# Kernel optimization log

Measured on AMD Instinct MI355X. Metric: run time of the kernel, lower is better.

Reference implementation:

```python
import jax, jax.numpy as jnp
import numpy as np

N_NODES = 100000
N_EDGES = 1600000
IN_FEATS = 128
OUT_FEATS = 256
K = 32


def setup_inputs() -> dict:
    key = jax.random.key(0)
    ks = jax.random.split(key, 8)
    feat = jax.random.normal(ks[0], (N_NODES, IN_FEATS), dtype=jnp.float32)
    # MaxK sparsified activations: nonnegative values (post-ReLU top-k)
    topk_values = jax.random.uniform(ks[1], (N_NODES, K), dtype=jnp.float32)
    topk_indices = jax.random.randint(ks[2], (N_NODES, K), 0, IN_FEATS, dtype=jnp.int32)
    # CSR expanded to COO: sorted row ids emulate indptr ordering
    row = jnp.sort(jax.random.randint(ks[3], (N_EDGES,), 0, N_NODES, dtype=jnp.int32))
    col = jax.random.randint(ks[4], (N_EDGES,), 0, N_NODES, dtype=jnp.int32)
    # in-degrees clamped to min 1.0, as in set_graph_data
    deg = jax.ops.segment_sum(jnp.ones((N_EDGES,), jnp.float32), row, num_segments=N_NODES)
    degrees = jnp.maximum(deg, 1.0)
    gain = float(np.sqrt(2.0))  # calculate_gain('relu')
    bnd_n = gain * np.sqrt(6.0 / (IN_FEATS + OUT_FEATS))
    W_neigh = jax.random.uniform(ks[5], (IN_FEATS, OUT_FEATS), jnp.float32, -bnd_n, bnd_n)
    W_self = jax.random.uniform(ks[6], (IN_FEATS, OUT_FEATS), jnp.float32, -bnd_n, bnd_n)
    bnd_b = 1.0 / np.sqrt(IN_FEATS)
    b_self = jax.random.uniform(ks[7], (OUT_FEATS,), jnp.float32, -bnd_b, bnd_b)
    return {"feat": feat, "topk_values": topk_values, "topk_indices": topk_indices,
            "row": row, "col": col, "degrees": degrees,
            "W_neigh": W_neigh, "W_self": W_self, "b_self": b_self}


def reference(feat, topk_values, topk_indices, row, col, degrees, W_neigh, W_self, b_self):
    n = feat.shape[0]
    # Scatter top-k sparse features back to dense [N, in_feats]
    # (real top-k indices are unique per row, so add == set; add is deterministic)
    rows = jnp.arange(n, dtype=jnp.int32)[:, None]
    x_sparse = jnp.zeros((n, IN_FEATS), feat.dtype).at[rows, topk_indices].add(topk_values)
    # CSR SpMM with all-ones edge values + degree normalization (mean aggregation)
    gathered = x_sparse[col]                                  # [E, in_feats]
    agg = jax.ops.segment_sum(gathered, row, num_segments=n)  # [N, in_feats]
    agg = agg / degrees[:, None]
    # lin_before_mp is False (in_feats <= out_feats): linear after aggregation
    h_neigh = agg @ W_neigh                                    # [N, out_feats]
    rst = feat @ W_self + b_self + h_neigh
    return rst
```

## Files before the change

### kernel.cpp

```cpp
#include <hip/hip_runtime.h>
#include <hip/hip_bf16.h>
#include <stdint.h>

#define IN_FEATS 128
#define OUT_FEATS 256
#define TOPK 32
#define BM 128
#define BN 128
#define BK 32
#define AL 40
#define KTOT 256

typedef float f32x4 __attribute__((ext_vector_type(4)));
typedef short bf16x8 __attribute__((ext_vector_type(8)));

__device__ __forceinline__ unsigned short f2bf(float x) {
    unsigned u = __float_as_uint(x);
    u += 0x7FFFu + ((u >> 16) & 1u);
    return (unsigned short)(u >> 16);
}

__global__ void k_scatter(const float* __restrict__ vals, const int* __restrict__ idxs,
                          unsigned short* __restrict__ xsp, int n_nodes) {
    __shared__ float lds[2 * IN_FEATS];
    int t = threadIdx.x;
    int n0 = blockIdx.x * 2;
    lds[t] = 0.f;
    __syncthreads();
    if (t < 2 * TOPK) {
        int h = t >> 5;
        int k = t & 31;
        int n = n0 + h;
        if (n < n_nodes) {
            float v = vals[(size_t)n * TOPK + k];
            int ix = idxs[(size_t)n * TOPK + k];
            atomicAdd(&lds[h * IN_FEATS + ix], v);
        }
    }
    __syncthreads();
    int h2 = t >> 7;
    int f = t & 127;
    int n = n0 + h2;
    if (n < n_nodes) xsp[(size_t)n * IN_FEATS + f] = f2bf(lds[t]);
}

__global__ void k_weights(const float* __restrict__ Wn, const float* __restrict__ Ws,
                          unsigned short* __restrict__ WT) {
    int idx = blockIdx.x * 256 + threadIdx.x;
    int n = idx >> 8;
    int k = idx & 255;
    float v = (k < IN_FEATS) ? Wn[(size_t)k * OUT_FEATS + n]
                             : Ws[(size_t)(k - IN_FEATS) * OUT_FEATS + n];
    WT[idx] = f2bf(v);
}

__global__ void k_indptr(const int* __restrict__ row, int* __restrict__ indptr,
                         int n_nodes, int n_edges) {
    int e = blockIdx.x * 256 + threadIdx.x;
    if (e >= n_edges) return;
    int r = row[e];
    int rp = (e == 0) ? -1 : row[e - 1];
    for (int x = rp + 1; x <= r; ++x) indptr[x] = e;
    if (e == n_edges - 1)
        for (int x = r + 1; x <= n_nodes; ++x) indptr[x] = n_edges;
}

__global__ __launch_bounds__(256) void k_aggregate(
    const unsigned short* __restrict__ xsp,
    const int* __restrict__ indptr, const int* __restrict__ col,
    unsigned short* __restrict__ agg, int n_nodes) {
    int t = threadIdx.x;
    int node = blockIdx.x * 4 + (t >> 6);
    if (node >= n_nodes) return;
    int lane = t & 63;
    int eg = lane >> 4, fi = lane & 15;
    int e0 = indptr[node], e1 = indptr[node + 1];

    float acc[8] = {0.f, 0.f, 0.f, 0.f, 0.f, 0.f, 0.f, 0.f};
    int elast = (e1 > e0) ? (e1 - 1) : e0;
    for (int base = e0; base < e1; base += 8) {
        int ea = base + eg;
        int eb = base + 4 + eg;
        float sa = (ea < e1) ? 1.f : 0.f;
        float sb = (eb < e1) ? 1.f : 0.f;
        int ca = col[ea < elast ? ea : elast];
        int cb = col[eb < elast ? eb : elast];
        uint4 ua = *(const uint4*)(xsp + (size_t)ca * IN_FEATS + fi * 8);
        uint4 ub = *(const uint4*)(xsp + (size_t)cb * IN_FEATS + fi * 8);
        unsigned pa[4] = {ua.x, ua.y, ua.z, ua.w};
        unsigned pb[4] = {ub.x, ub.y, ub.z, ub.w};
#pragma unroll
        for (int i = 0; i < 4; ++i) {
            acc[2 * i]     = fmaf(sa, __uint_as_float(pa[i] << 16), acc[2 * i]);
            acc[2 * i + 1] = fmaf(sa, __uint_as_float(pa[i] & 0xFFFF0000u), acc[2 * i + 1]);
            acc[2 * i]     = fmaf(sb, __uint_as_float(pb[i] << 16), acc[2 * i]);
            acc[2 * i + 1] = fmaf(sb, __uint_as_float(pb[i] & 0xFFFF0000u), acc[2 * i + 1]);
        }
    }
#pragma unroll
    for (int i = 0; i < 8; ++i) {
        acc[i] += __shfl_down(acc[i], 16, 64);
        acc[i] += __shfl_down(acc[i], 32, 64);
    }
    if (eg == 0) {
        int cnt = e1 - e0;
        float inv = 1.0f / (float)(cnt > 0 ? cnt : 1);
        unsigned o[4];
#pragma unroll
        for (int i = 0; i < 4; ++i) {
            unsigned lo = f2bf(acc[2 * i] * inv);
            unsigned hi = f2bf(acc[2 * i + 1] * inv);
            o[i] = lo | (hi << 16);
        }
        *(uint4*)(agg + (size_t)node * IN_FEATS + fi * 8) = *(uint4*)&o[0];
    }
}

__global__ __launch_bounds__(256) void k_gemm(
    const unsigned short* __restrict__ agg,
    const float* __restrict__ feat,
    const unsigned short* __restrict__ WT,
    const float* __restrict__ bias,
    float* __restrict__ out, int n_nodes) {
    __shared__ __align__(16) unsigned short Ash[BM * AL];
    __shared__ __align__(16) unsigned short Bsh[BN * AL];
    int t = threadIdx.x;
    int m0 = blockIdx.x * BM;
    int n0 = blockIdx.y * BN;
    int lane = t & 63;
    int w = t >> 6;
    int wr = w >> 1, wc = w & 1;
    int lrow = lane & 15, quad = lane >> 4;

    f32x4 acc[4][4];
    for (int i = 0; i < 4; ++i)
        for (int j = 0; j < 4; ++j)
            acc[i][j] = (f32x4){0.f, 0.f, 0.f, 0.f};

    for (int kk = 0; kk < KTOT; kk += BK) {
        for (int pass = 0; pass < 2; ++pass) {
            int g = t + pass * 256;
            int rowi = g >> 2;
            int q = g & 3;
            int gk = kk + q * 8;
            int node = m0 + rowi;
            if (node >= n_nodes) node = n_nodes - 1;
            uint4 v;
            if (kk < IN_FEATS) {
                v = *(const uint4*)(agg + (size_t)node * IN_FEATS + gk);
            } else {
                const float* fp = feat + (size_t)node * IN_FEATS + (gk - IN_FEATS);
                float4 f0 = *(const float4*)fp;
                float4 f1 = *(const float4*)(fp + 4);
                v.x = (unsigned)f2bf(f0.x) | ((unsigned)f2bf(f0.y) << 16);
                v.y = (unsigned)f2bf(f0.z) | ((unsigned)f2bf(f0.w) << 16);
                v.z = (unsigned)f2bf(f1.x) | ((unsigned)f2bf(f1.y) << 16);
                v.w = (unsigned)f2bf(f1.z) | ((unsigned)f2bf(f1.w) << 16);
            }
            *(uint4*)&Ash[rowi * AL + q * 8] = v;

            uint4 bv = *(const uint4*)(WT + (size_t)(n0 + rowi) * KTOT + gk);
            *(uint4*)&Bsh[rowi * AL + q * 8] = bv;
        }
        __syncthreads();

        bf16x8 af[4], bfr[4];
        for (int mi = 0; mi < 4; ++mi)
            af[mi] = *(const bf16x8*)&Ash[(wr * 64 + mi * 16 + lrow) * AL + quad * 8];
        for (int ni = 0; ni < 4; ++ni)
            bfr[ni] = *(const bf16x8*)&Bsh[(wc * 64 + ni * 16 + lrow) * AL + quad * 8];
        for (int mi = 0; mi < 4; ++mi)
            for (int ni = 0; ni < 4; ++ni)
                acc[mi][ni] = __builtin_amdgcn_mfma_f32_16x16x32_bf16(
                    af[mi], bfr[ni], acc[mi][ni], 0, 0, 0);
        __syncthreads();
    }

    for (int mi = 0; mi < 4; ++mi) {
        int gm = m0 + wr * 64 + mi * 16 + quad * 4;
        for (int ni = 0; ni < 4; ++ni) {
            int go = n0 + wc * 64 + ni * 16 + lrow;
            float b = bias[go];
            for (int r = 0; r < 4; ++r) {
                int node = gm + r;
                if (node < n_nodes)
                    out[(size_t)node * OUT_FEATS + go] = acc[mi][ni][r] + b;
            }
        }
    }
}

extern "C" void kernel_launch(void* const* d_in, const int* in_sizes, int n_in,
                              void* d_out, int out_size, void* d_ws, size_t ws_size,
                              hipStream_t stream) {
    const float* feat = (const float*)d_in[0];
    const float* tkv  = (const float*)d_in[1];
    const int*   tki  = (const int*)d_in[2];
    const int*   row  = (const int*)d_in[3];
    const int*   col  = (const int*)d_in[4];
    const float* Wn   = (const float*)d_in[6];
    const float* Ws   = (const float*)d_in[7];
    const float* bias = (const float*)d_in[8];
    float* out = (float*)d_out;

    int n_nodes = in_sizes[5];
    int n_edges = in_sizes[3];

    unsigned short* xsp = (unsigned short*)d_ws;
    unsigned short* agg = xsp + (size_t)n_nodes * IN_FEATS;
    unsigned short* WT  = agg + (size_t)n_nodes * IN_FEATS;
    int* indptr = (int*)(WT + (size_t)OUT_FEATS * KTOT);

    k_scatter<<<(n_nodes + 1) / 2, 256, 0, stream>>>(tkv, tki, xsp, n_nodes);
    k_weights<<<256, 256, 0, stream>>>(Wn, Ws, WT);
    k_indptr<<<(n_edges + 255) / 256, 256, 0, stream>>>(row, indptr, n_nodes, n_edges);
    k_aggregate<<<(n_nodes + 3) / 4, 256, 0, stream>>>(xsp, indptr, col, agg, n_nodes);
    dim3 g3((n_nodes + BM - 1) / BM, OUT_FEATS / BN);
    k_gemm<<<g3, 256, 0, stream>>>(agg, feat, WT, bias, out, n_nodes);
}
```

Before: 304.3 us.

## Stage concatenated bf16 A matrix and use direct global-to-LDS loads in GEMM

The feat-to-bf16 conversion moves into the aggregation kernel, which writes a concatenated [agg | feat] bf16 matrix of row stride 256. The GEMM then loads A and B tiles with global_load_lds straight into XOR-swizzled LDS at BK=64, replacing register-staged loads, in-kernel conversion and padded LDS rows. This is meant to cut GEMM load instructions and fp32 feat traffic repeated across both N-blocks. In exchange it adds an extra bf16 write and read of feat through the workspace.

```diff
diff --git a/kernel.cpp b/kernel.cpp
--- a/kernel.cpp
+++ b/kernel.cpp
@@ -1,5 +1,4 @@
 #include <hip/hip_runtime.h>
-#include <hip/hip_bf16.h>
 #include <stdint.h>
 
 #define IN_FEATS 128
@@ -7,8 +6,7 @@
 #define TOPK 32
 #define BM 128
 #define BN 128
-#define BK 32
-#define AL 40
+#define BK 64
 #define KTOT 256
 
 typedef float f32x4 __attribute__((ext_vector_type(4)));
@@ -18,6 +16,12 @@
     unsigned u = __float_as_uint(x);
     u += 0x7FFFu + ((u >> 16) & 1u);
     return (unsigned short)(u >> 16);
+}
+
+__device__ __forceinline__ void gload16(const void* g, void* l) {
+    __builtin_amdgcn_global_load_lds(
+        (const __attribute__((address_space(1))) unsigned*)g,
+        (__attribute__((address_space(3))) unsigned*)l, 16, 0, 0);
 }
 
 __global__ void k_scatter(const float* __restrict__ vals, const int* __restrict__ idxs,
@@ -67,8 +71,9 @@
 
 __global__ __launch_bounds__(256) void k_aggregate(
     const unsigned short* __restrict__ xsp,
+    const float* __restrict__ feat,
     const int* __restrict__ indptr, const int* __restrict__ col,
-    unsigned short* __restrict__ agg, int n_nodes) {
+    unsigned short* __restrict__ Acat, int n_nodes) {
     int t = threadIdx.x;
     int node = blockIdx.x * 4 + (t >> 6);
     if (node >= n_nodes) return;
@@ -112,18 +117,20 @@
             unsigned hi = f2bf(acc[2 * i + 1] * inv);
             o[i] = lo | (hi << 16);
         }
-        *(uint4*)(agg + (size_t)node * IN_FEATS + fi * 8) = *(uint4*)&o[0];
-    }
+        *(uint4*)(Acat + (size_t)node * KTOT + fi * 8) = *(uint4*)&o[0];
+    }
+    float2 fv = *(const float2*)(feat + (size_t)node * IN_FEATS + lane * 2);
+    unsigned pk = (unsigned)f2bf(fv.x) | ((unsigned)f2bf(fv.y) << 16);
+    *(unsigned*)(Acat + (size_t)node * KTOT + IN_FEATS + lane * 2) = pk;
 }
 
 __global__ __launch_bounds__(256) void k_gemm(
-    const unsigned short* __restrict__ agg,
-    const float* __restrict__ feat,
+    const unsigned short* __restrict__ Acat,
     const unsigned short* __restrict__ WT,
     const float* __restrict__ bias,
     float* __restrict__ out, int n_nodes) {
-    __shared__ __align__(16) unsigned short Ash[BM * AL];
-    __shared__ __align__(16) unsigned short Bsh[BN * AL];
+    __shared__ __align__(16) unsigned short Ash[BM * BK];
+    __shared__ __align__(16) unsigned short Bsh[BN * BK];
     int t = threadIdx.x;
     int m0 = blockIdx.x * BM;
     int n0 = blockIdx.y * BN;
@@ -133,54 +140,58 @@
     int lrow = lane & 15, quad = lane >> 4;
 
     f32x4 acc[4][4];
+#pragma unroll
     for (int i = 0; i < 4; ++i)
+#pragma unroll
         for (int j = 0; j < 4; ++j)
             acc[i][j] = (f32x4){0.f, 0.f, 0.f, 0.f};
 
     for (int kk = 0; kk < KTOT; kk += BK) {
-        for (int pass = 0; pass < 2; ++pass) {
-            int g = t + pass * 256;
-            int rowi = g >> 2;
-            int q = g & 3;
-            int gk = kk + q * 8;
-            int node = m0 + rowi;
-            if (node >= n_nodes) node = n_nodes - 1;
-            uint4 v;
-            if (kk < IN_FEATS) {
-                v = *(const uint4*)(agg + (size_t)node * IN_FEATS + gk);
-            } else {
-                const float* fp = feat + (size_t)node * IN_FEATS + (gk - IN_FEATS);
-                float4 f0 = *(const float4*)fp;
-                float4 f1 = *(const float4*)(fp + 4);
-                v.x = (unsigned)f2bf(f0.x) | ((unsigned)f2bf(f0.y) << 16);
-                v.y = (unsigned)f2bf(f0.z) | ((unsigned)f2bf(f0.w) << 16);
-                v.z = (unsigned)f2bf(f1.x) | ((unsigned)f2bf(f1.y) << 16);
-                v.w = (unsigned)f2bf(f1.z) | ((unsigned)f2bf(f1.w) << 16);
+#pragma unroll
+        for (int p = 0; p < 4; ++p) {
+            int c = p * 256 + t;
+            int row = c >> 3;
+            int q = (c & 7) ^ (row & 7);
+            int nodeA = m0 + row;
+            if (nodeA >= n_nodes) nodeA = n_nodes - 1;
+            gload16(Acat + (size_t)nodeA * KTOT + kk + q * 8, &Ash[(size_t)c * 8]);
+            gload16(WT + (size_t)(n0 + row) * KTOT + kk + q * 8, &Bsh[(size_t)c * 8]);
+        }
+        __syncthreads();
+
+#pragma unroll
+        for (int ks = 0; ks < 2; ++ks) {
+            bf16x8 af[4], bfr[4];
+#pragma unroll
+            for (int mi = 0; mi < 4; ++mi) {
+                int r = wr * 64 + mi * 16 + lrow;
+                int q = (ks * 4 + quad) ^ (r & 7);
+                af[mi] = *(const bf16x8*)&Ash[(r * 8 + q) * 8];
             }
-            *(uint4*)&Ash[rowi * AL + q * 8] = v;
-
-            uint4 bv = *(const uint4*)(WT + (size_t)(n0 + rowi) * KTOT + gk);
-            *(uint4*)&Bsh[rowi * AL + q * 8] = bv;
+#pragma unroll
+            for (int ni = 0; ni < 4; ++ni) {
+                int r = wc * 64 + ni * 16 + lrow;
+                int q = (ks * 4 + quad) ^ (r & 7);
+                bfr[ni] = *(const bf16x8*)&Bsh[(r * 8 + q) * 8];
+            }
+#pragma unroll
+            for (int mi = 0; mi < 4; ++mi)
+#pragma unroll
+                for (int ni = 0; ni < 4; ++ni)
+                    acc[mi][ni] = __builtin_amdgcn_mfma_f32_16x16x32_bf16(
+                        af[mi], bfr[ni], acc[mi][ni], 0, 0, 0);
         }
         __syncthreads();
-
-        bf16x8 af[4], bfr[4];
-        for (int mi = 0; mi < 4; ++mi)
-            af[mi] = *(const bf16x8*)&Ash[(wr * 64 + mi * 16 + lrow) * AL + quad * 8];
-        for (int ni = 0; ni < 4; ++ni)
-            bfr[ni] = *(const bf16x8*)&Bsh[(wc * 64 + ni * 16 + lrow) * AL + quad * 8];
-        for (int mi = 0; mi < 4; ++mi)
-            for (int ni = 0; ni < 4; ++ni)
-                acc[mi][ni] = __builtin_amdgcn_mfma_f32_16x16x32_bf16(
-                    af[mi], bfr[ni], acc[mi][ni], 0, 0, 0);
-        __syncthreads();
-    }
-
+    }
+
+#pragma unroll
     for (int mi = 0; mi < 4; ++mi) {
         int gm = m0 + wr * 64 + mi * 16 + quad * 4;
+#pragma unroll
         for (int ni = 0; ni < 4; ++ni) {
             int go = n0 + wc * 64 + ni * 16 + lrow;
             float b = bias[go];
+#pragma unroll
             for (int r = 0; r < 4; ++r) {
                 int node = gm + r;
                 if (node < n_nodes)
@@ -206,15 +217,15 @@
     int n_nodes = in_sizes[5];
     int n_edges = in_sizes[3];
 
-    unsigned short* xsp = (unsigned short*)d_ws;
-    unsigned short* agg = xsp + (size_t)n_nodes * IN_FEATS;
-    unsigned short* WT  = agg + (size_t)n_nodes * IN_FEATS;
+    unsigned short* xsp  = (unsigned short*)d_ws;
+    unsigned short* Acat = xsp + (size_t)n_nodes * IN_FEATS;
+    unsigned short* WT   = Acat + (size_t)n_nodes * KTOT;
     int* indptr = (int*)(WT + (size_t)OUT_FEATS * KTOT);
 
     k_scatter<<<(n_nodes + 1) / 2, 256, 0, stream>>>(tkv, tki, xsp, n_nodes);
     k_weights<<<256, 256, 0, stream>>>(Wn, Ws, WT);
     k_indptr<<<(n_edges + 255) / 256, 256, 0, stream>>>(row, indptr, n_nodes, n_edges);
-    k_aggregate<<<(n_nodes + 3) / 4, 256, 0, stream>>>(xsp, indptr, col, agg, n_nodes);
+    k_aggregate<<<(n_nodes + 3) / 4, 256, 0, stream>>>(xsp, feat, indptr, col, Acat, n_nodes);
     dim3 g3((n_nodes + BM - 1) / BM, OUT_FEATS / BN);
-    k_gemm<<<g3, 256, 0, stream>>>(agg, feat, WT, bias, out, n_nodes);
-}
+    k_gemm<<<g3, 256, 0, stream>>>(Acat, WT, bias, out, n_nodes);
+}
```

After: 313.5 us. 1.03x slower.
